# Performance work log

Measured on AMD Instinct MI355X. Metric: run time of the kernel, lower is better.

## Reference

```python
import jax, jax.numpy as jnp
import numpy as np

N_NODES = 50000
N_EDGES = 1600000
D = 128  # input_dim == hidden_dim


def glorot(key, shape):
    lim = float(np.sqrt(6.0 / (shape[0] + shape[1])))
    return jax.random.uniform(key, shape, jnp.float32, -lim, lim)


def setup_inputs() -> dict:
    key = jax.random.key(0)
    ks = jax.random.split(key, 10)
    x = jax.random.normal(ks[0], (N_NODES, D), jnp.float32)
    edge_index = jax.random.randint(ks[1], (2, N_EDGES), 0, N_NODES, jnp.int64)
    edge_attr = jax.random.normal(ks[2], (N_EDGES, D), jnp.float32)
    # SAGEConv params per layer: lin_l (W,b), lin_r (W, no bias)
    W1l = glorot(ks[3], (D, D)); b1l = jnp.zeros((D,), jnp.float32)
    W1r = glorot(ks[4], (D, D))
    W2l = glorot(ks[5], (D, D)); b2l = jnp.zeros((D,), jnp.float32)
    W2r = glorot(ks[6], (D, D))
    return {"x": x, "edge_index": edge_index, "edge_attr": edge_attr,
            "W1l": W1l, "b1l": b1l, "W1r": W1r,
            "W2l": W2l, "b2l": b2l, "W2r": W2r}


def sage_layer(z, src, dst, edge_attr, Wl, bl, Wr):
    # message: gather x_j, add edge_attr, relu  -> [E, D]
    msg = jax.nn.relu(z[src] + edge_attr)
    # mean aggregation at destination nodes
    agg = jax.ops.segment_sum(msg, dst, num_segments=N_NODES)
    cnt = jax.ops.segment_sum(jnp.ones((dst.shape[0], 1), z.dtype), dst,
                              num_segments=N_NODES)
    agg = agg / jnp.maximum(cnt, 1.0)
    # lin_l(agg) + lin_r(x) (root weight, no bias on lin_r)
    return agg @ Wl + bl + z @ Wr


def reference(x, edge_index, edge_attr, W1l, b1l, W1r, W2l, b2l, W2r):
    src, dst = edge_index[0], edge_index[1]
    z = sage_layer(x, src, dst, edge_attr, W1l, b1l, W1r)
    z = jax.nn.relu(z)  # activation between layers; dropout=0, normalize='none'
    z = sage_layer(z, src, dst, edge_attr, W2l, b2l, W2r)
    return z
```

## Files before the change

### kernel.cpp

```cpp
#include <hip/hip_runtime.h>

#define D 128

typedef __attribute__((ext_vector_type(8))) short bf16x8;
typedef __attribute__((ext_vector_type(4))) float f32x4;

__device__ inline unsigned short f2bf(float f) {
    union { float f; unsigned u; } v; v.f = f;
    unsigned r = v.u + 0x7FFF + ((v.u >> 16) & 1);
    return (unsigned short)(r >> 16);
}
__device__ inline float bf2f(unsigned short h) {
    union { unsigned u; float f; } v; v.u = ((unsigned)h) << 16; return v.f;
}


__global__ __launch_bounds__(256) void castx_kernel(const float* __restrict__ x,
                                                    unsigned short* __restrict__ xb, int n4) {
    int i = blockIdx.x * 256 + threadIdx.x;
    if (i < n4) {
        float4 v = reinterpret_cast<const float4*>(x)[i];
        ushort4 r;
        r.x = f2bf(v.x); r.y = f2bf(v.y); r.z = f2bf(v.z); r.w = f2bf(v.w);
        reinterpret_cast<ushort4*>(xb)[i] = r;
    }
}

__global__ __launch_bounds__(256) void wcast_kernel(const float* __restrict__ W1l,
                                                    const float* __restrict__ W1r,
                                                    const float* __restrict__ W2l,
                                                    const float* __restrict__ W2r,
                                                    unsigned short* __restrict__ Wt1,
                                                    unsigned short* __restrict__ Wt2) {
    int c = blockIdx.x, k = threadIdx.x;
    float v1 = (k < 128) ? W1l[k * 128 + c] : W1r[(k - 128) * 128 + c];
    float v2 = (k < 128) ? W2l[k * 128 + c] : W2r[(k - 128) * 128 + c];
    Wt1[c * 256 + k] = f2bf(v1);
    Wt2[c * 256 + k] = f2bf(v2);
}


__global__ __launch_bounds__(256) void count_kernel(const int* __restrict__ dst,
                                                    int* __restrict__ cnt, int E) {
    int e = blockIdx.x * 256 + threadIdx.x;
    if (e < E) atomicAdd(&cnt[dst[e]], 1);
}

__global__ __launch_bounds__(256) void psum_kernel(const int* __restrict__ cnt,
                                                   int* __restrict__ bsum, int n) {
    __shared__ int wsh[4];
    int b = blockIdx.x, tid = threadIdx.x;
    int i0 = b * 1024 + tid * 4;
    int s = 0;
    #pragma unroll
    for (int j = 0; j < 4; ++j) { int i = i0 + j; if (i < n) s += cnt[i]; }
    #pragma unroll
    for (int d = 1; d < 64; d <<= 1) s += __shfl_xor(s, d, 64);
    if ((tid & 63) == 0) wsh[tid >> 6] = s;
    __syncthreads();
    if (tid == 0) bsum[b] = wsh[0] + wsh[1] + wsh[2] + wsh[3];
}

__global__ __launch_bounds__(64) void bscan_kernel(const int* __restrict__ bsum,
                                                   int* __restrict__ bpre, int nb) {
    int t = threadIdx.x;
    int v = (t < nb) ? bsum[t] : 0;
    int sc = v;
    #pragma unroll
    for (int d = 1; d < 64; d <<= 1) { int u = __shfl_up(sc, d, 64); if (t >= d) sc += u; }
    if (t < nb) bpre[t] = sc - v;
}

__global__ __launch_bounds__(256) void fscan_kernel(const int* __restrict__ cnt,
                                                    const int* __restrict__ bpre,
                                                    int* __restrict__ off,
                                                    int* __restrict__ cursor, int n) {
    __shared__ int wsum[4];
    int b = blockIdx.x, tid = threadIdx.x;
    int lane = tid & 63, wv = tid >> 6;
    int i0 = b * 1024 + tid * 4;
    int v[4]; int s = 0;
    #pragma unroll
    for (int j = 0; j < 4; ++j) { int i = i0 + j; v[j] = (i < n) ? cnt[i] : 0; s += v[j]; }
    int sc = s;
    #pragma unroll
    for (int d = 1; d < 64; d <<= 1) { int u = __shfl_up(sc, d, 64); if (lane >= d) sc += u; }
    if (lane == 63) wsum[wv] = sc;
    __syncthreads();
    int wp = 0;
    for (int j = 0; j < wv; ++j) wp += wsum[j];
    int base = bpre[b] + wp + sc - s;
    #pragma unroll
    for (int j = 0; j < 4; ++j) {
        int i = i0 + j;
        if (i < n) { cursor[i] = base; off[i + 1] = base + v[j]; }
        base += v[j];
    }
    if (b == 0 && tid == 0) off[0] = 0;
}

__global__ __launch_bounds__(256) void fill_kernel(const int* __restrict__ src,
                                                   const int* __restrict__ dst,
                                                   int* __restrict__ cursor,
                                                   int2* __restrict__ pairs, int E) {
    int e = blockIdx.x * 256 + threadIdx.x;
    if (e < E) {
        int d = dst[e];
        int slot = atomicAdd(&cursor[d], 1);
        pairs[slot] = make_int2(src[e], e);
    }
}


__global__ __launch_bounds__(256) void aggregate_kernel(const unsigned short* __restrict__ featb,
                                                        const float* __restrict__ ea,
                                                        const int* __restrict__ off,
                                                        const long long* __restrict__ pairs,
                                                        unsigned short* __restrict__ aggb,
                                                        int N) {
    int nd = blockIdx.x * 4 + (threadIdx.x >> 6);
    if (nd >= N) return;
    int t = threadIdx.x & 63;
    int half = t >> 5, l32 = t & 31;
    int s = off[nd], e = off[nd + 1];
    float a0 = 0.f, a1 = 0.f, a2 = 0.f, a3 = 0.f;

    for (int b = s; b < e; b += 64) {
        int cnt = min(64, e - b);
        long long prl = (b + t < e) ? __builtin_nontemporal_load(&pairs[b + t]) : 0LL;
        int psrc = (int)(prl & 0xFFFFFFFFLL);
        int peid = (int)((unsigned long long)prl >> 32);

        auto fetch = [&](int idx, float4& ev, ushort4& xv) {
            int sidx = __shfl(psrc, idx, 64);
            int eidx = __shfl(peid, idx, 64);
            const float* ep = &ea[(size_t)eidx * D + l32 * 4];
            ev = make_float4(__builtin_nontemporal_load(ep + 0),
                             __builtin_nontemporal_load(ep + 1),
                             __builtin_nontemporal_load(ep + 2),
                             __builtin_nontemporal_load(ep + 3));
            xv = *reinterpret_cast<const ushort4*>(&featb[(size_t)sidx * D + l32 * 4]);
        };
        auto accum = [&](const float4& ev, const ushort4& xv) {
            a0 += fmaxf(bf2f(xv.x) + ev.x, 0.f);
            a1 += fmaxf(bf2f(xv.y) + ev.y, 0.f);
            a2 += fmaxf(bf2f(xv.z) + ev.z, 0.f);
            a3 += fmaxf(bf2f(xv.w) + ev.w, 0.f);
        };

        int p = 0;
        for (; p + 4 <= cnt; p += 4) {
            float4 e0; ushort4 x0; fetch(p + half, e0, x0);
            float4 e1; ushort4 x1; fetch(p + 2 + half, e1, x1);
            accum(e0, x0);
            accum(e1, x1);
        }
        if (p + 2 <= cnt) {
            float4 e0; ushort4 x0; fetch(p + half, e0, x0);
            accum(e0, x0);
            p += 2;
        }
        if (p < cnt) {
            float4 e0; ushort4 x0; fetch(p, e0, x0);
            if (half == 0) accum(e0, x0);
        }
    }

    a0 += __shfl_xor(a0, 32, 64);
    a1 += __shfl_xor(a1, 32, 64);
    a2 += __shfl_xor(a2, 32, 64);
    a3 += __shfl_xor(a3, 32, 64);
    int deg = e - s;
    float inv = 1.f / (float)(deg > 0 ? deg : 1);
    if (half == 0) {
        ushort4 r;
        r.x = f2bf(a0 * inv); r.y = f2bf(a1 * inv);
        r.z = f2bf(a2 * inv); r.w = f2bf(a3 * inv);
        *reinterpret_cast<ushort4*>(&aggb[(size_t)nd * D + l32 * 4]) = r;
    }
}


template <int RELU, int OUT_BF16>
__global__ __launch_bounds__(256) void gemm_mfma_kernel(const unsigned short* __restrict__ A1,
                                                        const unsigned short* __restrict__ A2,
                                                        const unsigned short* __restrict__ Wt,
                                                        const float* __restrict__ bias,
                                                        float* __restrict__ outf,
                                                        unsigned short* __restrict__ outb,
                                                        int MT) {
    int tid = threadIdx.x;
    int w = tid >> 6;
    int l = tid & 63;
    int lr = l & 15;
    int lg = l >> 4;
    int c0 = w * 32;

    bf16x8 bfr[2][8];
    #pragma unroll
    for (int t = 0; t < 2; ++t)
        #pragma unroll
        for (int kc = 0; kc < 8; ++kc)
            bfr[t][kc] = *reinterpret_cast<const bf16x8*>(
                &Wt[(size_t)(c0 + t * 16 + lr) * 256 + kc * 32 + lg * 8]);

    for (int mt = blockIdx.x; mt < MT; mt += gridDim.x) {
        int r0 = mt * 16;
        f32x4 acc0 = {0.f, 0.f, 0.f, 0.f};
        f32x4 acc1 = {0.f, 0.f, 0.f, 0.f};
        #pragma unroll
        for (int kc = 0; kc < 8; ++kc) {
            const unsigned short* Ap = (kc < 4) ? A1 : A2;
            int k = (kc & 3) * 32 + lg * 8;
            bf16x8 af = *reinterpret_cast<const bf16x8*>(&Ap[(size_t)(r0 + lr) * D + k]);
            acc0 = __builtin_amdgcn_mfma_f32_16x16x32_bf16(af, bfr[0][kc], acc0, 0, 0, 0);
            acc1 = __builtin_amdgcn_mfma_f32_16x16x32_bf16(af, bfr[1][kc], acc1, 0, 0, 0);
        }
        #pragma unroll
        for (int t = 0; t < 2; ++t) {
            const f32x4& a = t ? acc1 : acc0;
            int col = c0 + t * 16 + lr;
            float bv = bias[col];
            #pragma unroll
            for (int r = 0; r < 4; ++r) {
                int row = r0 + lg * 4 + r;
                float v = a[r] + bv;
                if (RELU) v = fmaxf(v, 0.f);
                if (OUT_BF16) outb[(size_t)row * D + col] = f2bf(v);
                else outf[(size_t)row * D + col] = v;
            }
        }
    }
}

extern "C" void kernel_launch(void* const* d_in, const int* in_sizes, int n_in,
                              void* d_out, int out_size, void* d_ws, size_t ws_size,
                              hipStream_t stream) {
    const float* x   = (const float*)d_in[0];
    const int*   ei  = (const int*)d_in[1];
    const float* ea  = (const float*)d_in[2];
    const float* W1l = (const float*)d_in[3];
    const float* b1l = (const float*)d_in[4];
    const float* W1r = (const float*)d_in[5];
    const float* W2l = (const float*)d_in[6];
    const float* b2l = (const float*)d_in[7];
    const float* W2r = (const float*)d_in[8];
    float* out = (float*)d_out;

    const int N = in_sizes[0] / D;
    const int E = in_sizes[1] / 2;
    const int* src = ei;
    const int* dst = ei + E;

    char* ws = (char*)d_ws;
    size_t o = 0;
    auto alloc = [&](size_t bytes) -> void* {
        void* p = ws + o;
        o = (o + bytes + 255) & ~(size_t)255;
        return p;
    };
    int*   cnt    = (int*)alloc((size_t)N * 4);
    int*   off    = (int*)alloc((size_t)(N + 1) * 4);
    int*   cursor = (int*)alloc((size_t)N * 4);
    int*   bsum   = (int*)alloc(256 * 4);
    int*   bpre   = (int*)alloc(256 * 4);
    int2*  pairs  = (int2*)alloc((size_t)E * 8);
    unsigned short* xb   = (unsigned short*)alloc((size_t)N * D * 2);
    unsigned short* z1b  = (unsigned short*)alloc((size_t)N * D * 2);
    unsigned short* aggb = (unsigned short*)alloc((size_t)N * D * 2);
    unsigned short* Wt1  = (unsigned short*)alloc(128 * 256 * 2);
    unsigned short* Wt2  = (unsigned short*)alloc(128 * 256 * 2);
    (void)ws_size; (void)n_in; (void)out_size;

    const int MT = N / 16;
    const int NB = (N + 1023) / 1024;
    const int AGB = (N + 3) / 4;

    castx_kernel<<<(N * D / 4 + 255) / 256, 256, 0, stream>>>(x, xb, N * D / 4);
    wcast_kernel<<<128, 256, 0, stream>>>(W1l, W1r, W2l, W2r, Wt1, Wt2);

    (void)hipMemsetAsync(cnt, 0, (size_t)N * 4, stream);
    count_kernel<<<(E + 255) / 256, 256, 0, stream>>>(dst, cnt, E);
    psum_kernel<<<NB, 256, 0, stream>>>(cnt, bsum, N);
    bscan_kernel<<<1, 64, 0, stream>>>(bsum, bpre, NB);
    fscan_kernel<<<NB, 256, 0, stream>>>(cnt, bpre, off, cursor, N);
    fill_kernel<<<(E + 255) / 256, 256, 0, stream>>>(src, dst, cursor, pairs, E);

    aggregate_kernel<<<AGB, 256, 0, stream>>>(xb, ea, off, (const long long*)pairs, aggb, N);
    gemm_mfma_kernel<1, 1><<<1024, 256, 0, stream>>>(aggb, xb, Wt1, b1l, nullptr, z1b, MT);

    aggregate_kernel<<<AGB, 256, 0, stream>>>(z1b, ea, off, (const long long*)pairs, aggb, N);
    gemm_mfma_kernel<0, 0><<<1024, 256, 0, stream>>>(aggb, z1b, Wt2, b2l, out, nullptr, MT);
}
```

Measured before the change: 603.7 us.

## Cache edge attributes as bf16 in CSR order for second aggregation; widen GEMM tile

The first aggregation pass writes a bf16 copy of edge_attr in destination-sorted order, and the second pass reads that compact, sequential copy instead of gathering the fp32 edge features. This halves edge-feature traffic in layer two and makes its access contiguous, at the cost of an extra ~400MB write in layer one. It also unrolls the edge loop to 8 in-flight fetches and changes the GEMM to 32-row tiles with bounds checks. The risks are lower precision on edge_attr in layer two and the added write cost in layer one.

```diff
diff --git a/kernel.cpp b/kernel.cpp
--- a/kernel.cpp
+++ b/kernel.cpp
@@ -4,6 +4,7 @@
 
 typedef __attribute__((ext_vector_type(8))) short bf16x8;
 typedef __attribute__((ext_vector_type(4))) float f32x4;
+typedef __attribute__((ext_vector_type(4))) unsigned short u16x4;
 
 __device__ inline unsigned short f2bf(float f) {
     union { float f; unsigned u; } v; v.f = f;
@@ -112,8 +113,10 @@
 }
 
 
+template <int WRITE_EAB, int EA_BF16>
 __global__ __launch_bounds__(256) void aggregate_kernel(const unsigned short* __restrict__ featb,
                                                         const float* __restrict__ ea,
+                                                        unsigned short* __restrict__ eab,
                                                         const int* __restrict__ off,
                                                         const long long* __restrict__ pairs,
                                                         unsigned short* __restrict__ aggb,
@@ -128,40 +131,63 @@
     for (int b = s; b < e; b += 64) {
         int cnt = min(64, e - b);
         long long prl = (b + t < e) ? __builtin_nontemporal_load(&pairs[b + t]) : 0LL;
-        int psrc = (int)(prl & 0xFFFFFFFFLL);
-        int peid = (int)((unsigned long long)prl >> 32);
-
-        auto fetch = [&](int idx, float4& ev, ushort4& xv) {
+        int psrc = (int)prl;
+        int peid = (int)(prl >> 32);
+
+        auto fetch = [&](int idx, f32x4& ev, u16x4& xv) {
             int sidx = __shfl(psrc, idx, 64);
-            int eidx = __shfl(peid, idx, 64);
-            const float* ep = &ea[(size_t)eidx * D + l32 * 4];
-            ev = make_float4(__builtin_nontemporal_load(ep + 0),
-                             __builtin_nontemporal_load(ep + 1),
-                             __builtin_nontemporal_load(ep + 2),
-                             __builtin_nontemporal_load(ep + 3));
-            xv = *reinterpret_cast<const ushort4*>(&featb[(size_t)sidx * D + l32 * 4]);
+            int q = b + idx;
+            if (EA_BF16) {
+                u16x4 eb = __builtin_nontemporal_load(
+                    reinterpret_cast<const u16x4*>(&eab[(size_t)q * D + l32 * 4]));
+                ev[0] = bf2f(eb[0]); ev[1] = bf2f(eb[1]);
+                ev[2] = bf2f(eb[2]); ev[3] = bf2f(eb[3]);
+            } else {
+                int eidx = __shfl(peid, idx, 64);
+                ev = __builtin_nontemporal_load(
+                    reinterpret_cast<const f32x4*>(&ea[(size_t)eidx * D + l32 * 4]));
+                if (WRITE_EAB) {
+                    u16x4 wv;
+                    wv[0] = f2bf(ev[0]); wv[1] = f2bf(ev[1]);
+                    wv[2] = f2bf(ev[2]); wv[3] = f2bf(ev[3]);
+                    __builtin_nontemporal_store(wv,
+                        reinterpret_cast<u16x4*>(&eab[(size_t)q * D + l32 * 4]));
+                }
+            }
+            xv = *reinterpret_cast<const u16x4*>(&featb[(size_t)sidx * D + l32 * 4]);
         };
-        auto accum = [&](const float4& ev, const ushort4& xv) {
-            a0 += fmaxf(bf2f(xv.x) + ev.x, 0.f);
-            a1 += fmaxf(bf2f(xv.y) + ev.y, 0.f);
-            a2 += fmaxf(bf2f(xv.z) + ev.z, 0.f);
-            a3 += fmaxf(bf2f(xv.w) + ev.w, 0.f);
+        auto accum = [&](const f32x4& ev, const u16x4& xv) {
+            a0 += fmaxf(bf2f(xv[0]) + ev[0], 0.f);
+            a1 += fmaxf(bf2f(xv[1]) + ev[1], 0.f);
+            a2 += fmaxf(bf2f(xv[2]) + ev[2], 0.f);
+            a3 += fmaxf(bf2f(xv[3]) + ev[3], 0.f);
         };
 
         int p = 0;
-        for (; p + 4 <= cnt; p += 4) {
-            float4 e0; ushort4 x0; fetch(p + half, e0, x0);
-            float4 e1; ushort4 x1; fetch(p + 2 + half, e1, x1);
-            accum(e0, x0);
-            accum(e1, x1);
+        for (; p + 8 <= cnt; p += 8) {
+            f32x4 e0, e1, e2, e3; u16x4 x0, x1, x2, x3;
+            fetch(p + half, e0, x0);
+            fetch(p + 2 + half, e1, x1);
+            fetch(p + 4 + half, e2, x2);
+            fetch(p + 6 + half, e3, x3);
+            accum(e0, x0); accum(e1, x1); accum(e2, x2); accum(e3, x3);
+        }
+        if (p + 4 <= cnt) {
+            f32x4 e0, e1; u16x4 x0, x1;
+            fetch(p + half, e0, x0);
+            fetch(p + 2 + half, e1, x1);
+            accum(e0, x0); accum(e1, x1);
+            p += 4;
         }
         if (p + 2 <= cnt) {
-            float4 e0; ushort4 x0; fetch(p + half, e0, x0);
+            f32x4 e0; u16x4 x0;
+            fetch(p + half, e0, x0);
             accum(e0, x0);
             p += 2;
         }
         if (p < cnt) {
-            float4 e0; ushort4 x0; fetch(p, e0, x0);
+            f32x4 e0; u16x4 x0;
+            fetch(p, e0, x0);
             if (half == 0) accum(e0, x0);
         }
     }
@@ -188,7 +214,7 @@
                                                         const float* __restrict__ bias,
                                                         float* __restrict__ outf,
                                                         unsigned short* __restrict__ outb,
-                                                        int MT) {
+                                                        int MT, int N) {
     int tid = threadIdx.x;
     int w = tid >> 6;
     int l = tid & 63;
@@ -205,29 +231,41 @@
                 &Wt[(size_t)(c0 + t * 16 + lr) * 256 + kc * 32 + lg * 8]);
 
     for (int mt = blockIdx.x; mt < MT; mt += gridDim.x) {
-        int r0 = mt * 16;
-        f32x4 acc0 = {0.f, 0.f, 0.f, 0.f};
-        f32x4 acc1 = {0.f, 0.f, 0.f, 0.f};
+        int r0 = mt * 32;
+        f32x4 acc[2][2];
+        #pragma unroll
+        for (int tr = 0; tr < 2; ++tr)
+            #pragma unroll
+            for (int tc = 0; tc < 2; ++tc) acc[tr][tc] = {0.f, 0.f, 0.f, 0.f};
+
         #pragma unroll
         for (int kc = 0; kc < 8; ++kc) {
             const unsigned short* Ap = (kc < 4) ? A1 : A2;
             int k = (kc & 3) * 32 + lg * 8;
-            bf16x8 af = *reinterpret_cast<const bf16x8*>(&Ap[(size_t)(r0 + lr) * D + k]);
-            acc0 = __builtin_amdgcn_mfma_f32_16x16x32_bf16(af, bfr[0][kc], acc0, 0, 0, 0);
-            acc1 = __builtin_amdgcn_mfma_f32_16x16x32_bf16(af, bfr[1][kc], acc1, 0, 0, 0);
-        }
+            bf16x8 af0 = *reinterpret_cast<const bf16x8*>(&Ap[(size_t)(r0 + lr) * D + k]);
+            bf16x8 af1 = *reinterpret_cast<const bf16x8*>(&Ap[(size_t)(r0 + 16 + lr) * D + k]);
+            acc[0][0] = __builtin_amdgcn_mfma_f32_16x16x32_bf16(af0, bfr[0][kc], acc[0][0], 0, 0, 0);
+            acc[1][0] = __builtin_amdgcn_mfma_f32_16x16x32_bf16(af1, bfr[0][kc], acc[1][0], 0, 0, 0);
+            acc[0][1] = __builtin_amdgcn_mfma_f32_16x16x32_bf16(af0, bfr[1][kc], acc[0][1], 0, 0, 0);
+            acc[1][1] = __builtin_amdgcn_mfma_f32_16x16x32_bf16(af1, bfr[1][kc], acc[1][1], 0, 0, 0);
+        }
+
         #pragma unroll
-        for (int t = 0; t < 2; ++t) {
-            const f32x4& a = t ? acc1 : acc0;
-            int col = c0 + t * 16 + lr;
+        for (int tc = 0; tc < 2; ++tc) {
+            int col = c0 + tc * 16 + lr;
             float bv = bias[col];
             #pragma unroll
-            for (int r = 0; r < 4; ++r) {
-                int row = r0 + lg * 4 + r;
-                float v = a[r] + bv;
-                if (RELU) v = fmaxf(v, 0.f);
-                if (OUT_BF16) outb[(size_t)row * D + col] = f2bf(v);
-                else outf[(size_t)row * D + col] = v;
+            for (int tr = 0; tr < 2; ++tr) {
+                #pragma unroll
+                for (int r = 0; r < 4; ++r) {
+                    int row = r0 + tr * 16 + lg * 4 + r;
+                    if (row < N) {
+                        float v = acc[tr][tc][r] + bv;
+                        if (RELU) v = fmaxf(v, 0.f);
+                        if (OUT_BF16) outb[(size_t)row * D + col] = f2bf(v);
+                        else outf[(size_t)row * D + col] = v;
+                    }
+                }
             }
         }
     }
@@ -249,6 +287,7 @@
 
     const int N = in_sizes[0] / D;
     const int E = in_sizes[1] / 2;
+    const int NP = (N + 31) & ~31;
     const int* src = ei;
     const int* dst = ei + E;
 
@@ -265,14 +304,15 @@
     int*   bsum   = (int*)alloc(256 * 4);
     int*   bpre   = (int*)alloc(256 * 4);
     int2*  pairs  = (int2*)alloc((size_t)E * 8);
-    unsigned short* xb   = (unsigned short*)alloc((size_t)N * D * 2);
-    unsigned short* z1b  = (unsigned short*)alloc((size_t)N * D * 2);
-    unsigned short* aggb = (unsigned short*)alloc((size_t)N * D * 2);
+    unsigned short* eab  = (unsigned short*)alloc((size_t)E * D * 2);
+    unsigned short* xb   = (unsigned short*)alloc((size_t)NP * D * 2);
+    unsigned short* z1b  = (unsigned short*)alloc((size_t)NP * D * 2);
+    unsigned short* aggb = (unsigned short*)alloc((size_t)NP * D * 2);
     unsigned short* Wt1  = (unsigned short*)alloc(128 * 256 * 2);
     unsigned short* Wt2  = (unsigned short*)alloc(128 * 256 * 2);
     (void)ws_size; (void)n_in; (void)out_size;
 
-    const int MT = N / 16;
+    const int MT = (N + 31) / 32;
     const int NB = (N + 1023) / 1024;
     const int AGB = (N + 3) / 4;
 
@@ -286,9 +326,11 @@
     fscan_kernel<<<NB, 256, 0, stream>>>(cnt, bpre, off, cursor, N);
     fill_kernel<<<(E + 255) / 256, 256, 0, stream>>>(src, dst, cursor, pairs, E);
 
-    aggregate_kernel<<<AGB, 256, 0, stream>>>(xb, ea, off, (const long long*)pairs, aggb, N);
-    gemm_mfma_kernel<1, 1><<<1024, 256, 0, stream>>>(aggb, xb, Wt1, b1l, nullptr, z1b, MT);
-
-    aggregate_kernel<<<AGB, 256, 0, stream>>>(z1b, ea, off, (const long long*)pairs, aggb, N);
-    gemm_mfma_kernel<0, 0><<<1024, 256, 0, stream>>>(aggb, z1b, Wt2, b2l, out, nullptr, MT);
-}
+    aggregate_kernel<1, 0><<<AGB, 256, 0, stream>>>(xb, ea, eab, off,
+                                                    (const long long*)pairs, aggb, N);
+    gemm_mfma_kernel<1, 1><<<1024, 256, 0, stream>>>(aggb, xb, Wt1, b1l, nullptr, z1b, MT, N);
+
+    aggregate_kernel<0, 1><<<AGB, 256, 0, stream>>>(z1b, nullptr, eab, off,
+                                                    (const long long*)pairs, aggb, N);
+    gemm_mfma_kernel<0, 0><<<1024, 256, 0, stream>>>(aggb, z1b, Wt2, b2l, out, nullptr, MT, N);
+}
```

Measured after the change: 612.6 us. About the same (+1.5%).
